# Optimization experiments

Hardware: AMD Instinct MI355X
Metric: run time of the kernel (lower is better)

The kernel has to match this reference:

```python
import jax, jax.numpy as jnp
import numpy as np

B, T, N, E = 8, 80, 50000, 1600000
DT = 0.02  # integration time step (seconds)


def setup_inputs() -> dict:
    key = jax.random.key(0)
    ks = jax.random.split(key, 8)
    # stimulus over time: (batch, timesteps, n_nodes)
    x = jax.random.normal(ks[0], (B, T, N), dtype=jnp.float32)
    # node params (RestingPotential ~ N(0.5, 0.05); TimeConstant = 0.05)
    bias = 0.5 + 0.05 * jax.random.normal(ks[1], (N,), dtype=jnp.float32)
    time_const = jnp.full((N,), 0.05, dtype=jnp.float32)
    # edge params: sign in {-1,+1}, lognormal-ish counts, small non-negative strengths
    sign = jnp.where(jax.random.uniform(ks[2], (E,)) < 0.5, -1.0, 1.0).astype(jnp.float32)
    syn_count = jax.random.uniform(ks[3], (E,), dtype=jnp.float32, minval=0.5, maxval=5.0)
    syn_strength = jax.random.uniform(ks[4], (E,), dtype=jnp.float32, minval=0.0, maxval=0.02)
    source_indices = jax.random.randint(ks[5], (E,), 0, N, dtype=jnp.int32)
    target_indices = jax.random.randint(ks[6], (E,), 0, N, dtype=jnp.int32)
    return dict(x=x, bias=bias, time_const=time_const, sign=sign,
                syn_count=syn_count, syn_strength=syn_strength,
                source_indices=source_indices, target_indices=target_indices)


def reference(x, bias, time_const, sign, syn_count, syn_strength,
              source_indices, target_indices):
    """PPNeuronIGRSynapses dynamics with Euler integration.

    v_{t+1} = v_t + dt/max(tau, dt) * (-v_t + bias + scatter_add(w * relu(v_src)) + x_t)
    with w = sign * syn_count * clamp_nonneg(syn_strength).
    Returns activities of shape (B, T, N).
    """
    n_nodes = bias.shape[0]
    # derived edge weight (syn_strength clamped non-negative per clamp config)
    weight = sign * syn_count * jnp.maximum(syn_strength, 0.0)  # (E,)
    inv_tau = 1.0 / jnp.maximum(time_const, DT)                 # (N,)
    v0 = jnp.broadcast_to(bias, (x.shape[0], n_nodes))          # initial state = bias

    def step(v, x_t):
        # gather source activity across edges, relu activation, weight -> edge currents
        cur = weight * jnp.maximum(v[:, source_indices], 0.0)   # (B, E)
        # scatter-add edge currents into target nodes
        i_syn = jnp.zeros_like(v).at[:, target_indices].add(cur)  # (B, N)
        v_next = v + DT * inv_tau * (-v + bias + i_syn + x_t)
        return v_next, v_next

    _, vs = jax.lax.scan(step, v0, jnp.swapaxes(x, 0, 1))  # vs: (T, B, N)
    return jnp.swapaxes(vs, 0, 1)  # (B, T, N)
```

## Files before the change

kernel.cpp:

```cpp
#include <hip/hip_runtime.h>
#include <hip/hip_bf16.h>

#define NN 50000
#define NE 1600000
#define NB 8
#define NT 80
#define TN ((size_t)NT * NN)
#define DT_F 0.02f

#define LPN 8
#define KPRE 6

#define BKT_SHIFT 11
#define NBKT 25
#define NBKT_PAD 32
#define BKT_CAP 72000
#define ACHUNK 2048
#define BPB 64


__global__ void init_nodes_kernel(const float* __restrict__ bias,
                                  const float* __restrict__ tc,
                                  ushort* __restrict__ r0,
                                  float* __restrict__ alpha,
                                  int* __restrict__ cnt,
                                  int* __restrict__ bucket_cursor) {
  int n = blockIdx.x * blockDim.x + threadIdx.x;
  if (n >= NN) return;
  float b = bias[n];
  __hip_bfloat16 rb = __float2bfloat16(fmaxf(b, 0.f));
  ushort rbu = *(ushort*)&rb;
#pragma unroll
  for (int j = 0; j < NB; ++j) r0[(size_t)n * NB + j] = rbu;
  alpha[n] = DT_F / fmaxf(tc[n], DT_F);
  cnt[n] = 0;
  if (n < NBKT_PAD) bucket_cursor[n] = 0;
}

__global__ void hist_kernel(const int* __restrict__ tgt, int* __restrict__ cnt) {
  int e = blockIdx.x * blockDim.x + threadIdx.x;
  if (e >= NE) return;
  atomicAdd(&cnt[tgt[e]], 1);
}

__global__ void fill_kernel(const int* __restrict__ src, const int* __restrict__ tgt,
                            const float* __restrict__ sgn, const float* __restrict__ syn_cnt,
                            const float* __restrict__ syn_str,
                            int* __restrict__ cursor,
                            unsigned int* __restrict__ csr) {
  int e = blockIdx.x * blockDim.x + threadIdx.x;
  if (e >= NE) return;
  int t = tgt[e];
  float w = sgn[e] * syn_cnt[e] * fmaxf(syn_str[e], 0.f);
  __hip_bfloat16 wh = __float2bfloat16(w);
  unsigned int wb = *(ushort*)&wh;
  int pos = atomicAdd(&cursor[t], 1);
  csr[pos] = (unsigned int)src[e] | (wb << 16);
}

__global__ __launch_bounds__(256) void fillA_kernel(
    const int* __restrict__ src, const int* __restrict__ tgt,
    const float* __restrict__ sgn, const float* __restrict__ syn_cnt,
    const float* __restrict__ syn_str,
    int* __restrict__ node_cnt,
    int* __restrict__ bucket_cursor,
    unsigned long long* __restrict__ bkt) {
  __shared__ int bcnt[NBKT];
  __shared__ int bbase[NBKT];
  __shared__ int bpos[NBKT + 1];
  __shared__ unsigned long long stage[ACHUNK];
  __shared__ unsigned char stageb[ACHUNK];

  const int tid = threadIdx.x;
  const int base = blockIdx.x * ACHUNK;
#define EPT (ACHUNK / 256)

  int b_[EPT], off_[EPT];
  unsigned long long ent_[EPT];
  bool val_[EPT];
#pragma unroll
  for (int k = 0; k < EPT; ++k) {
    int e = base + k * 256 + tid;
    val_[k] = e < NE;
    b_[k] = 0;
    ent_[k] = 0;
    if (val_[k]) {
      int s = src[e];
      int t = tgt[e];
      float w = sgn[e] * syn_cnt[e] * fmaxf(syn_str[e], 0.f);
      atomicAdd(&node_cnt[t], 1);
      b_[k] = t >> BKT_SHIFT;
      unsigned int packed = (unsigned int)s | ((unsigned int)(t & ((1 << BKT_SHIFT) - 1)) << 16);
      ent_[k] = ((unsigned long long)(unsigned int)__float_as_int(w) << 32) | packed;
    }
  }

  if (tid < NBKT) bcnt[tid] = 0;
  __syncthreads();
#pragma unroll
  for (int k = 0; k < EPT; ++k)
    if (val_[k]) off_[k] = atomicAdd(&bcnt[b_[k]], 1);
  __syncthreads();
  if (tid == 0) {
    int run = 0;
    for (int i = 0; i < NBKT; ++i) { bpos[i] = run; run += bcnt[i]; }
    bpos[NBKT] = run;
  }
  __syncthreads();
  if (tid < NBKT) bbase[tid] = atomicAdd(&bucket_cursor[tid], bcnt[tid]);
#pragma unroll
  for (int k = 0; k < EPT; ++k) {
    if (val_[k]) {
      int slot = bpos[b_[k]] + off_[k];
      stage[slot] = ent_[k];
      stageb[slot] = (unsigned char)b_[k];
    }
  }
  __syncthreads();
  const int tot = bpos[NBKT];
  for (int i = tid; i < tot; i += 256) {
    int bb = stageb[i];
    int dst = bbase[bb] + (i - bpos[bb]);
    if (dst < BKT_CAP)
      bkt[(size_t)bb * BKT_CAP + dst] = stage[i];
  }
#undef EPT
}

__global__ __launch_bounds__(256) void fillB_kernel(
    const unsigned long long* __restrict__ bkt,
    const int* __restrict__ bucket_cursor,
    int* __restrict__ cursor,
    unsigned int* __restrict__ csr) {
  const int b = blockIdx.x & (NBKT_PAD - 1);
  if (b >= NBKT) return;
  const int j = blockIdx.x >> 5;
  const int count = bucket_cursor[b];
  const unsigned long long* mybkt = bkt + (size_t)b * BKT_CAP;
  for (int i = j * 256 + threadIdx.x; i < count; i += BPB * 256) {
    unsigned long long ent = mybkt[i];
    unsigned int packed = (unsigned int)ent;
    float w = __int_as_float((int)(ent >> 32));
    unsigned int s = packed & 0xFFFF;
    int t = (b << BKT_SHIFT) + ((packed >> 16) & ((1 << BKT_SHIFT) - 1));
    __hip_bfloat16 wh = __float2bfloat16(w);
    unsigned int wb = *(ushort*)&wh;
    int pos = atomicAdd(&cursor[t], 1);
    csr[pos] = s | (wb << 16);
  }
}

#define SCAN_BS 256
#define SCAN_NB ((NN + SCAN_BS - 1) / SCAN_BS)

__global__ __launch_bounds__(SCAN_BS) void scan1_kernel(
    const int* __restrict__ cnt, int* __restrict__ escan,
    int* __restrict__ partials) {
  __shared__ int buf[2][SCAN_BS];
  const int tid = threadIdx.x;
  const int i = blockIdx.x * SCAN_BS + tid;
  int v = (i < NN) ? cnt[i] : 0;
  int sel = 0;
  buf[0][tid] = v;
  __syncthreads();
#pragma unroll
  for (int off = 1; off < SCAN_BS; off <<= 1) {
    int s = buf[sel][tid];
    if (tid >= off) s += buf[sel][tid - off];
    buf[sel ^ 1][tid] = s;
    sel ^= 1;
    __syncthreads();
  }
  int incl = buf[sel][tid];
  if (i < NN) escan[i] = incl - v;
  if (tid == SCAN_BS - 1) partials[blockIdx.x] = incl;
}

__global__ __launch_bounds__(SCAN_BS) void scan2_kernel(
    int* __restrict__ partials, int* __restrict__ row_ptr) {
  __shared__ int buf[2][SCAN_BS];
  const int tid = threadIdx.x;
  int v = (tid < SCAN_NB) ? partials[tid] : 0;
  int sel = 0;
  buf[0][tid] = v;
  __syncthreads();
#pragma unroll
  for (int off = 1; off < SCAN_BS; off <<= 1) {
    int s = buf[sel][tid];
    if (tid >= off) s += buf[sel][tid - off];
    buf[sel ^ 1][tid] = s;
    sel ^= 1;
    __syncthreads();
  }
  int incl = buf[sel][tid];
  if (tid < SCAN_NB) partials[tid] = incl - v;
  if (tid == SCAN_BS - 1) row_ptr[NN] = incl;
}

__global__ __launch_bounds__(SCAN_BS) void scan3_kernel(
    const int* __restrict__ escan, const int* __restrict__ partials,
    int* __restrict__ row_ptr, int* __restrict__ cursor) {
  const int i = blockIdx.x * SCAN_BS + threadIdx.x;
  if (i >= NN) return;
  int r = escan[i] + partials[blockIdx.x];
  row_ptr[i] = r;
  cursor[i] = r;
}

__global__ __launch_bounds__(256) void step1_kernel(
    const int* __restrict__ row_ptr,
    const unsigned int* __restrict__ csr,
    const ushort* __restrict__ r_old,
    ushort* __restrict__ r_new,
    const float* __restrict__ x_t,
    const float* __restrict__ vprev,
    const float* __restrict__ bias,
    const float* __restrict__ alpha,
    float* __restrict__ out_t,
    int first) {
  int gid = blockIdx.x * blockDim.x + threadIdx.x;
  int node = gid >> 3;
  int lane = gid & 7;
  if (node >= NN) return;

  int e0 = row_ptr[node];
  int e1 = row_ptr[node + 1];
  int mybase = e0 + lane;
  int rem = e1 - mybase;
  int cnt = rem > 0 ? ((rem + LPN - 1) >> 3) : 0;

  float a = alpha[node];
  float bs = bias[node];
  size_t idx = (size_t)node * NB + lane;
  size_t boff = (size_t)lane * TN + node;
  float xv = __builtin_nontemporal_load(&x_t[boff]);
  float v = bs;
  if (!first) v = vprev[boff];

  int soff[KPRE];
  float wk[KPRE];
#pragma unroll
  for (int k = 0; k < KPRE; ++k) {
    unsigned int c = (k < cnt) ? csr[mybase + (k << 3)] : 0u;
    soff[k] = (int)(c & 0xFFFFu) << 4;
    wk[k] = __uint_as_float(c & 0xFFFF0000u);
  }

  uint4 rv[KPRE];
#pragma unroll
  for (int k = 0; k < KPRE; ++k) {
    if (k < cnt)
      rv[k] = *(const uint4*)((const char*)r_old + soff[k]);
    else
      rv[k] = make_uint4(0, 0, 0, 0);
  }

  float acc[NB];
#pragma unroll
  for (int j = 0; j < NB; ++j) acc[j] = 0.f;

#pragma unroll
  for (int k = 0; k < KPRE; ++k) {
    float w = wk[k];
    acc[0] += w * __uint_as_float(rv[k].x << 16);
    acc[1] += w * __uint_as_float(rv[k].x & 0xffff0000u);
    acc[2] += w * __uint_as_float(rv[k].y << 16);
    acc[3] += w * __uint_as_float(rv[k].y & 0xffff0000u);
    acc[4] += w * __uint_as_float(rv[k].z << 16);
    acc[5] += w * __uint_as_float(rv[k].z & 0xffff0000u);
    acc[6] += w * __uint_as_float(rv[k].w << 16);
    acc[7] += w * __uint_as_float(rv[k].w & 0xffff0000u);
  }

  for (int e = mybase + (KPRE << 3); e < e1; e += LPN) {
    unsigned int c = csr[e];
    uint4 r8 = *(const uint4*)((const char*)r_old + ((size_t)(c & 0xFFFFu) << 4));
    float w = __uint_as_float(c & 0xFFFF0000u);
    acc[0] += w * __uint_as_float(r8.x << 16);
    acc[1] += w * __uint_as_float(r8.x & 0xffff0000u);
    acc[2] += w * __uint_as_float(r8.y << 16);
    acc[3] += w * __uint_as_float(r8.y & 0xffff0000u);
    acc[4] += w * __uint_as_float(r8.z << 16);
    acc[5] += w * __uint_as_float(r8.z & 0xffff0000u);
    acc[6] += w * __uint_as_float(r8.w << 16);
    acc[7] += w * __uint_as_float(r8.w & 0xffff0000u);
  }

#pragma unroll
  for (int off = 4; off; off >>= 1) {
#pragma unroll
    for (int j = 0; j < NB; ++j) {
      float t = __shfl_xor(acc[j], off);
      acc[j] = (((lane ^ j) & off) == 0) ? acc[j] + t : acc[j];
    }
  }
  float r = acc[0];
#pragma unroll
  for (int j = 1; j < NB; ++j) r = (lane == j) ? acc[j] : r;

  float vn = v + a * (bs - v + r + xv);
  __hip_bfloat16 rh = __float2bfloat16(fmaxf(vn, 0.f));
  r_new[idx] = *(ushort*)&rh;
  out_t[boff] = vn;
}


extern "C" void kernel_launch(void* const* d_in, const int* in_sizes, int n_in,
                              void* d_out, int out_size, void* d_ws, size_t ws_size,
                              hipStream_t stream) {
  const float* x        = (const float*)d_in[0];
  const float* bias     = (const float*)d_in[1];
  const float* tc       = (const float*)d_in[2];
  const float* sgn      = (const float*)d_in[3];
  const float* syn_cnt  = (const float*)d_in[4];
  const float* syn_str  = (const float*)d_in[5];
  const int*   src      = (const int*)d_in[6];
  const int*   tgt      = (const int*)d_in[7];
  float* out = (float*)d_out;

  char* p = (char*)d_ws;
  auto take = [&p](size_t bytes) {
    char* r = p;
    p += (bytes + 255) & ~(size_t)255;
    return (void*)r;
  };
  ushort* r_a      = (ushort*)take((size_t)NN * NB * sizeof(ushort));
  ushort* r_b      = (ushort*)take((size_t)NN * NB * sizeof(ushort));
  float*  alpha    = (float*)take((size_t)NN * sizeof(float));
  int*    row_ptr  = (int*)take(((size_t)NN + 1) * sizeof(int));
  int*    cnt      = (int*)take((size_t)NN * sizeof(int));
  int*    cursor   = (int*)take((size_t)NN * sizeof(int));
  int*    escan    = (int*)take((size_t)NN * sizeof(int));
  int*    partials = (int*)take((size_t)SCAN_NB * sizeof(int));
  int*    bcur     = (int*)take((size_t)NBKT_PAD * sizeof(int));
  unsigned int* csr = (unsigned int*)take((size_t)NE * sizeof(unsigned int));
  unsigned long long* bkt =
      (unsigned long long*)take((size_t)NBKT * BKT_CAP * sizeof(unsigned long long));
  const bool use_bucketed = ((size_t)(p - (char*)d_ws) <= ws_size);

  init_nodes_kernel<<<(NN + 255) / 256, 256, 0, stream>>>(bias, tc, r_a,
                                                          alpha, cnt, bcur);
  if (use_bucketed) {
    fillA_kernel<<<(NE + ACHUNK - 1) / ACHUNK, 256, 0, stream>>>(
        src, tgt, sgn, syn_cnt, syn_str, cnt, bcur, bkt);
    scan1_kernel<<<SCAN_NB, SCAN_BS, 0, stream>>>(cnt, escan, partials);
    scan2_kernel<<<1, SCAN_BS, 0, stream>>>(partials, row_ptr);
    scan3_kernel<<<SCAN_NB, SCAN_BS, 0, stream>>>(escan, partials, row_ptr, cursor);
    fillB_kernel<<<NBKT_PAD * BPB, 256, 0, stream>>>(bkt, bcur, cursor, csr);
  } else {
    hist_kernel<<<(NE + 255) / 256, 256, 0, stream>>>(tgt, cnt);
    scan1_kernel<<<SCAN_NB, SCAN_BS, 0, stream>>>(cnt, escan, partials);
    scan2_kernel<<<1, SCAN_BS, 0, stream>>>(partials, row_ptr);
    scan3_kernel<<<SCAN_NB, SCAN_BS, 0, stream>>>(escan, partials, row_ptr, cursor);
    fill_kernel<<<(NE + 255) / 256, 256, 0, stream>>>(src, tgt, sgn, syn_cnt,
                                                      syn_str, cursor, csr);
  }

  const int blocks = (NN * LPN + 255) / 256;
  const ushort* rin = r_a;
  ushort* rout = r_b;
  for (int t = 0; t < NT; ++t) {
    step1_kernel<<<blocks, 256, 0, stream>>>(
        row_ptr, csr, rin, rout,
        x + (size_t)t * NN,
        out + (size_t)(t > 0 ? t - 1 : 0) * NN,
        bias, alpha,
        out + (size_t)t * NN,
        t == 0 ? 1 : 0);
    ushort* tr = (ushort*)rin; rin = rout; rout = tr;
  }
}
```

Measured before the change: 1.123 ms.

## Store first 48 edges per node in lane-interleaved transposed slabs with per-lane counts

Edge lists are rebuilt so the first 48 incoming edges of each node go into six slabs laid out as [k][node][lane]. Each step-kernel lane then reads its k-th edge with fully coalesced loads and no row_ptr lookup. Per-lane edge counts are precomputed into a byte array, with nodes of more than 48 edges flagged to use an overflow CSR path. Alpha and bias are packed into one float2. The cost is a memset of the slab buffer, extra workspace, and a branchy overflow path for high-degree nodes.

```diff
diff --git a/kernel.cpp b/kernel.cpp
--- a/kernel.cpp
+++ b/kernel.cpp
@@ -9,12 +9,13 @@
 #define DT_F 0.02f
 
 #define LPN 8
-#define KPRE 6
+#define KP 6
+#define NN8 (NN * NB)
 
 #define BKT_SHIFT 11
 #define NBKT 25
 #define NBKT_PAD 32
-#define BKT_CAP 72000
+#define BKT_CAP 68000
 #define ACHUNK 2048
 #define BPB 64
 
@@ -22,7 +23,7 @@
 __global__ void init_nodes_kernel(const float* __restrict__ bias,
                                   const float* __restrict__ tc,
                                   ushort* __restrict__ r0,
-                                  float* __restrict__ alpha,
+                                  float2* __restrict__ ab,
                                   int* __restrict__ cnt,
                                   int* __restrict__ bucket_cursor) {
   int n = blockIdx.x * blockDim.x + threadIdx.x;
@@ -32,7 +33,7 @@
   ushort rbu = *(ushort*)&rb;
 #pragma unroll
   for (int j = 0; j < NB; ++j) r0[(size_t)n * NB + j] = rbu;
-  alpha[n] = DT_F / fmaxf(tc[n], DT_F);
+  ab[n] = make_float2(DT_F / fmaxf(tc[n], DT_F), b);
   cnt[n] = 0;
   if (n < NBKT_PAD) bucket_cursor[n] = 0;
 }
@@ -46,16 +47,21 @@
 __global__ void fill_kernel(const int* __restrict__ src, const int* __restrict__ tgt,
                             const float* __restrict__ sgn, const float* __restrict__ syn_cnt,
                             const float* __restrict__ syn_str,
-                            int* __restrict__ cursor,
-                            unsigned int* __restrict__ csr) {
+                            const int* __restrict__ row_ptr,
+                            int* __restrict__ cursor0,
+                            unsigned int* __restrict__ csrt,
+                            unsigned int* __restrict__ ovf) {
   int e = blockIdx.x * blockDim.x + threadIdx.x;
   if (e >= NE) return;
   int t = tgt[e];
   float w = sgn[e] * syn_cnt[e] * fmaxf(syn_str[e], 0.f);
   __hip_bfloat16 wh = __float2bfloat16(w);
-  unsigned int wb = *(ushort*)&wh;
-  int pos = atomicAdd(&cursor[t], 1);
-  csr[pos] = (unsigned int)src[e] | (wb << 16);
+  unsigned int entry = (unsigned int)src[e] | ((unsigned int)*(ushort*)&wh << 16);
+  int j = atomicAdd(&cursor0[t], 1);
+  if (j < 48)
+    csrt[(size_t)(j >> 3) * NN8 + t * 8 + (j & 7)] = entry;
+  else
+    ovf[row_ptr[t] + j] = entry;
 }
 
 __global__ __launch_bounds__(256) void fillA_kernel(
@@ -130,12 +136,14 @@
 __global__ __launch_bounds__(256) void fillB_kernel(
     const unsigned long long* __restrict__ bkt,
     const int* __restrict__ bucket_cursor,
-    int* __restrict__ cursor,
-    unsigned int* __restrict__ csr) {
+    const int* __restrict__ row_ptr,
+    int* __restrict__ cursor0,
+    unsigned int* __restrict__ csrt,
+    unsigned int* __restrict__ ovf) {
   const int b = blockIdx.x & (NBKT_PAD - 1);
   if (b >= NBKT) return;
   const int j = blockIdx.x >> 5;
-  const int count = bucket_cursor[b];
+  const int count = min(bucket_cursor[b], BKT_CAP);
   const unsigned long long* mybkt = bkt + (size_t)b * BKT_CAP;
   for (int i = j * 256 + threadIdx.x; i < count; i += BPB * 256) {
     unsigned long long ent = mybkt[i];
@@ -144,9 +152,12 @@
     unsigned int s = packed & 0xFFFF;
     int t = (b << BKT_SHIFT) + ((packed >> 16) & ((1 << BKT_SHIFT) - 1));
     __hip_bfloat16 wh = __float2bfloat16(w);
-    unsigned int wb = *(ushort*)&wh;
-    int pos = atomicAdd(&cursor[t], 1);
-    csr[pos] = s | (wb << 16);
+    unsigned int entry = s | ((unsigned int)*(ushort*)&wh << 16);
+    int jj = atomicAdd(&cursor0[t], 1);
+    if (jj < 48)
+      csrt[(size_t)(jj >> 3) * NN8 + t * 8 + (jj & 7)] = entry;
+    else
+      ovf[row_ptr[t] + jj] = entry;
   }
 }
 
@@ -199,23 +210,39 @@
 
 __global__ __launch_bounds__(SCAN_BS) void scan3_kernel(
     const int* __restrict__ escan, const int* __restrict__ partials,
-    int* __restrict__ row_ptr, int* __restrict__ cursor) {
+    const int* __restrict__ cnt,
+    int* __restrict__ row_ptr, int* __restrict__ cursor0,
+    unsigned long long* __restrict__ cnt8) {
   const int i = blockIdx.x * SCAN_BS + threadIdx.x;
   if (i >= NN) return;
-  int r = escan[i] + partials[blockIdx.x];
-  row_ptr[i] = r;
-  cursor[i] = r;
+  row_ptr[i] = escan[i] + partials[blockIdx.x];
+  cursor0[i] = 0;
+  int deg = cnt[i];
+  unsigned long long packed;
+  if (deg > 48) {
+    packed = 0xFFFFFFFFFFFFFFFFull;
+  } else {
+    packed = 0;
+#pragma unroll
+    for (int l = 0; l < 8; ++l) {
+      int c = (deg - l + 7) >> 3;
+      if (c < 0) c = 0;
+      packed |= (unsigned long long)(unsigned int)c << (8 * l);
+    }
+  }
+  cnt8[i] = packed;
 }
 
 __global__ __launch_bounds__(256) void step1_kernel(
+    const unsigned char* __restrict__ cnt8,
+    const unsigned int* __restrict__ csrt,
+    const unsigned int* __restrict__ ovf,
     const int* __restrict__ row_ptr,
-    const unsigned int* __restrict__ csr,
     const ushort* __restrict__ r_old,
     ushort* __restrict__ r_new,
     const float* __restrict__ x_t,
     const float* __restrict__ vprev,
-    const float* __restrict__ bias,
-    const float* __restrict__ alpha,
+    const float2* __restrict__ ab,
     float* __restrict__ out_t,
     int first) {
   int gid = blockIdx.x * blockDim.x + threadIdx.x;
@@ -223,34 +250,25 @@
   int lane = gid & 7;
   if (node >= NN) return;
 
-  int e0 = row_ptr[node];
-  int e1 = row_ptr[node + 1];
-  int mybase = e0 + lane;
-  int rem = e1 - mybase;
-  int cnt = rem > 0 ? ((rem + LPN - 1) >> 3) : 0;
-
-  float a = alpha[node];
-  float bs = bias[node];
-  size_t idx = (size_t)node * NB + lane;
+  unsigned char c8 = cnt8[gid];
+  float2 abv = ab[node];
   size_t boff = (size_t)lane * TN + node;
   float xv = __builtin_nontemporal_load(&x_t[boff]);
-  float v = bs;
+  float v = abv.y;
   if (!first) v = vprev[boff];
 
-  int soff[KPRE];
-  float wk[KPRE];
-#pragma unroll
-  for (int k = 0; k < KPRE; ++k) {
-    unsigned int c = (k < cnt) ? csr[mybase + (k << 3)] : 0u;
-    soff[k] = (int)(c & 0xFFFFu) << 4;
-    wk[k] = __uint_as_float(c & 0xFFFF0000u);
-  }
-
-  uint4 rv[KPRE];
-#pragma unroll
-  for (int k = 0; k < KPRE; ++k) {
+  unsigned int ce[KP];
+#pragma unroll
+  for (int k = 0; k < KP; ++k)
+    ce[k] = csrt[(size_t)k * NN8 + gid];
+
+  int cnt = (c8 == 255u) ? KP : (int)c8;
+
+  uint4 rv[KP];
+#pragma unroll
+  for (int k = 0; k < KP; ++k) {
     if (k < cnt)
-      rv[k] = *(const uint4*)((const char*)r_old + soff[k]);
+      rv[k] = *(const uint4*)((const char*)r_old + ((size_t)(ce[k] & 0xFFFFu) << 4));
     else
       rv[k] = make_uint4(0, 0, 0, 0);
   }
@@ -260,8 +278,8 @@
   for (int j = 0; j < NB; ++j) acc[j] = 0.f;
 
 #pragma unroll
-  for (int k = 0; k < KPRE; ++k) {
-    float w = wk[k];
+  for (int k = 0; k < KP; ++k) {
+    float w = __uint_as_float(ce[k] & 0xFFFF0000u);
     acc[0] += w * __uint_as_float(rv[k].x << 16);
     acc[1] += w * __uint_as_float(rv[k].x & 0xffff0000u);
     acc[2] += w * __uint_as_float(rv[k].y << 16);
@@ -272,18 +290,22 @@
     acc[7] += w * __uint_as_float(rv[k].w & 0xffff0000u);
   }
 
-  for (int e = mybase + (KPRE << 3); e < e1; e += LPN) {
-    unsigned int c = csr[e];
-    uint4 r8 = *(const uint4*)((const char*)r_old + ((size_t)(c & 0xFFFFu) << 4));
-    float w = __uint_as_float(c & 0xFFFF0000u);
-    acc[0] += w * __uint_as_float(r8.x << 16);
-    acc[1] += w * __uint_as_float(r8.x & 0xffff0000u);
-    acc[2] += w * __uint_as_float(r8.y << 16);
-    acc[3] += w * __uint_as_float(r8.y & 0xffff0000u);
-    acc[4] += w * __uint_as_float(r8.z << 16);
-    acc[5] += w * __uint_as_float(r8.z & 0xffff0000u);
-    acc[6] += w * __uint_as_float(r8.w << 16);
-    acc[7] += w * __uint_as_float(r8.w & 0xffff0000u);
+  if (c8 == 255u) {
+    int e0 = row_ptr[node];
+    int e1 = row_ptr[node + 1];
+    for (int e = e0 + 48 + lane; e < e1; e += LPN) {
+      unsigned int c = ovf[e];
+      uint4 r8 = *(const uint4*)((const char*)r_old + ((size_t)(c & 0xFFFFu) << 4));
+      float w = __uint_as_float(c & 0xFFFF0000u);
+      acc[0] += w * __uint_as_float(r8.x << 16);
+      acc[1] += w * __uint_as_float(r8.x & 0xffff0000u);
+      acc[2] += w * __uint_as_float(r8.y << 16);
+      acc[3] += w * __uint_as_float(r8.y & 0xffff0000u);
+      acc[4] += w * __uint_as_float(r8.z << 16);
+      acc[5] += w * __uint_as_float(r8.z & 0xffff0000u);
+      acc[6] += w * __uint_as_float(r8.w << 16);
+      acc[7] += w * __uint_as_float(r8.w & 0xffff0000u);
+    }
   }
 
 #pragma unroll
@@ -298,9 +320,9 @@
 #pragma unroll
   for (int j = 1; j < NB; ++j) r = (lane == j) ? acc[j] : r;
 
-  float vn = v + a * (bs - v + r + xv);
+  float vn = v + abv.x * (abv.y - v + r + xv);
   __hip_bfloat16 rh = __float2bfloat16(fmaxf(vn, 0.f));
-  r_new[idx] = *(ushort*)&rh;
+  r_new[(size_t)node * NB + lane] = *(ushort*)&rh;
   out_t[boff] = vn;
 }
 
@@ -326,45 +348,54 @@
   };
   ushort* r_a      = (ushort*)take((size_t)NN * NB * sizeof(ushort));
   ushort* r_b      = (ushort*)take((size_t)NN * NB * sizeof(ushort));
-  float*  alpha    = (float*)take((size_t)NN * sizeof(float));
+  float2* ab       = (float2*)take((size_t)NN * sizeof(float2));
   int*    row_ptr  = (int*)take(((size_t)NN + 1) * sizeof(int));
   int*    cnt      = (int*)take((size_t)NN * sizeof(int));
-  int*    cursor   = (int*)take((size_t)NN * sizeof(int));
+  int*    cursor0  = (int*)take((size_t)NN * sizeof(int));
   int*    escan    = (int*)take((size_t)NN * sizeof(int));
   int*    partials = (int*)take((size_t)SCAN_NB * sizeof(int));
   int*    bcur     = (int*)take((size_t)NBKT_PAD * sizeof(int));
-  unsigned int* csr = (unsigned int*)take((size_t)NE * sizeof(unsigned int));
+  unsigned long long* cnt8 =
+      (unsigned long long*)take((size_t)NN * sizeof(unsigned long long));
+  unsigned int* csrt = (unsigned int*)take((size_t)KP * NN8 * sizeof(unsigned int));
+  unsigned int* ovf  = (unsigned int*)take((size_t)NE * sizeof(unsigned int));
   unsigned long long* bkt =
       (unsigned long long*)take((size_t)NBKT * BKT_CAP * sizeof(unsigned long long));
   const bool use_bucketed = ((size_t)(p - (char*)d_ws) <= ws_size);
 
-  init_nodes_kernel<<<(NN + 255) / 256, 256, 0, stream>>>(bias, tc, r_a,
-                                                          alpha, cnt, bcur);
+  hipMemsetAsync(csrt, 0, (size_t)KP * NN8 * sizeof(unsigned int), stream);
+
+  init_nodes_kernel<<<(NN + 255) / 256, 256, 0, stream>>>(bias, tc, r_a, ab,
+                                                          cnt, bcur);
   if (use_bucketed) {
     fillA_kernel<<<(NE + ACHUNK - 1) / ACHUNK, 256, 0, stream>>>(
         src, tgt, sgn, syn_cnt, syn_str, cnt, bcur, bkt);
     scan1_kernel<<<SCAN_NB, SCAN_BS, 0, stream>>>(cnt, escan, partials);
     scan2_kernel<<<1, SCAN_BS, 0, stream>>>(partials, row_ptr);
-    scan3_kernel<<<SCAN_NB, SCAN_BS, 0, stream>>>(escan, partials, row_ptr, cursor);
-    fillB_kernel<<<NBKT_PAD * BPB, 256, 0, stream>>>(bkt, bcur, cursor, csr);
+    scan3_kernel<<<SCAN_NB, SCAN_BS, 0, stream>>>(escan, partials, cnt,
+                                                  row_ptr, cursor0, cnt8);
+    fillB_kernel<<<NBKT_PAD * BPB, 256, 0, stream>>>(bkt, bcur, row_ptr,
+                                                     cursor0, csrt, ovf);
   } else {
     hist_kernel<<<(NE + 255) / 256, 256, 0, stream>>>(tgt, cnt);
     scan1_kernel<<<SCAN_NB, SCAN_BS, 0, stream>>>(cnt, escan, partials);
     scan2_kernel<<<1, SCAN_BS, 0, stream>>>(partials, row_ptr);
-    scan3_kernel<<<SCAN_NB, SCAN_BS, 0, stream>>>(escan, partials, row_ptr, cursor);
+    scan3_kernel<<<SCAN_NB, SCAN_BS, 0, stream>>>(escan, partials, cnt,
+                                                  row_ptr, cursor0, cnt8);
     fill_kernel<<<(NE + 255) / 256, 256, 0, stream>>>(src, tgt, sgn, syn_cnt,
-                                                      syn_str, cursor, csr);
-  }
-
-  const int blocks = (NN * LPN + 255) / 256;
+                                                      syn_str, row_ptr, cursor0,
+                                                      csrt, ovf);
+  }
+
+  const int blocks = (NN8 + 255) / 256;
   const ushort* rin = r_a;
   ushort* rout = r_b;
   for (int t = 0; t < NT; ++t) {
     step1_kernel<<<blocks, 256, 0, stream>>>(
-        row_ptr, csr, rin, rout,
+        (const unsigned char*)cnt8, csrt, ovf, row_ptr, rin, rout,
         x + (size_t)t * NN,
         out + (size_t)(t > 0 ? t - 1 : 0) * NN,
-        bias, alpha,
+        ab,
         out + (size_t)t * NN,
         t == 0 ? 1 : 0);
     ushort* tr = (ushort*)rin; rin = rout; rout = tr;
```

Measured after the change: 1.113 ms. No clear change (-0.8%).
